# Optimization experiments

Measured on AMD Instinct MI355X. Metric: run time of the kernel, lower is better.

Reference implementation:

```python
import jax, jax.numpy as jnp
import numpy as np
from jax import lax

B, L, H, F, K, NBINS, MAXLEN = 32, 256, 256, 256, 3, 256, 2048
EPS = 1e-5


def _conv1d(x, w, b):
    # x: [B, L, Cin], w: [K, Cin, Cout] (torch Conv1d 'same' padding = (K-1)//2)
    pad = (w.shape[0] - 1) // 2
    y = lax.conv_general_dilated(x, w, (1,), [(pad, pad)],
                                 dimension_numbers=('NWC', 'WIO', 'NWC'))
    return y + b


def _layernorm(x, g, b):
    m = jnp.mean(x, axis=-1, keepdims=True)
    v = jnp.var(x, axis=-1, keepdims=True)
    return (x - m) * lax.rsqrt(v + EPS) * g + b


def _variance_predictor(x, i, w1, b1, g1, be1, w2, b2, g2, be2, wl, bl, mask):
    # conv -> relu -> LN -> conv -> relu -> LN -> linear -> squeeze -> masked_fill
    h = _layernorm(jax.nn.relu(_conv1d(x, w1[i], b1[i])), g1[i], be1[i])
    h = _layernorm(jax.nn.relu(_conv1d(h, w2[i], b2[i])), g2[i], be2[i])
    out = (h @ wl[i] + bl[i])[..., 0]          # [B, L]
    return jnp.where(mask, 0.0, out)


def _length_regulate(x, duration, max_len):
    # Vectorized replacement for the per-token expand/cat loop:
    # cumsum offsets + parallel gather into a padded buffer.
    cum = jnp.cumsum(duration, axis=1)          # [B, L]
    mel_len = cum[:, -1]                        # [B]
    t = jnp.arange(max_len)                     # [T]
    # phoneme index owning frame t: first position where cum > t
    idx = jax.vmap(lambda c: jnp.searchsorted(c, t, side='right'))(cum)  # [B, T]
    idx = jnp.minimum(idx, x.shape[1] - 1)
    out = jnp.take_along_axis(x, idx[:, :, None], axis=1)  # [B, T, H]
    valid = t[None, :] < mel_len[:, None]                   # [B, T]
    out = out * valid[:, :, None].astype(x.dtype)           # zero padding
    return out, mel_len, ~valid


def setup_inputs() -> dict:
    key = jax.random.key(0)
    ks = jax.random.split(key, 20)
    s = 1.0 / np.sqrt(H)
    inp = {
        'x': jax.random.normal(ks[0], (B, L, H), jnp.float32),
        'pitch_target': jax.random.normal(ks[1], (B, L), jnp.float32),
        'energy_target': jax.random.normal(ks[2], (B, L), jnp.float32),
        # stacked params for the 3 predictors: 0=duration, 1=pitch, 2=energy
        'w1': jax.random.normal(ks[3], (3, K, H, F), jnp.float32) * s,
        'b1': jnp.zeros((3, F), jnp.float32),
        'g1': jnp.ones((3, F), jnp.float32),
        'be1': jnp.zeros((3, F), jnp.float32),
        'w2': jax.random.normal(ks[4], (3, K, F, F), jnp.float32) * s,
        'b2': jnp.zeros((3, F), jnp.float32),
        'g2': jnp.ones((3, F), jnp.float32),
        'be2': jnp.zeros((3, F), jnp.float32),
        'wl': jax.random.normal(ks[5], (3, F, 1), jnp.float32) * s,
        'bl': jnp.zeros((3, 1), jnp.float32),
        'pitch_bins': jnp.linspace(-3.0, 3.0, NBINS - 1, dtype=jnp.float32),
        'energy_bins': jnp.linspace(-3.0, 3.0, NBINS - 1, dtype=jnp.float32),
        'pitch_emb': jax.random.normal(ks[6], (NBINS, H), jnp.float32),
        'energy_emb': jax.random.normal(ks[7], (NBINS, H), jnp.float32),
        'src_mask': jnp.zeros((B, L), bool),
        'duration_target': jax.random.randint(ks[8], (B, L), 0, 8),
        'max_len': MAXLEN,
    }
    return inp


def reference(x, pitch_target, energy_target,
              w1, b1, g1, be1, w2, b2, g2, be2, wl, bl,
              pitch_bins, energy_bins, pitch_emb, energy_emb,
              src_mask, duration_target, max_len):
    p = (w1, b1, g1, be1, w2, b2, g2, be2, wl, bl)
    log_duration_prediction = _variance_predictor(x, 0, *p, src_mask)
    # phoneme-level pitch (training path: target given -> bucketize + embed)
    pitch_prediction = _variance_predictor(x, 1, *p, src_mask)
    pitch_idx = jnp.searchsorted(pitch_bins, pitch_target, side='left')
    x = x + pitch_emb[pitch_idx]
    # phoneme-level energy (predictor sees x AFTER pitch embedding added)
    energy_prediction = _variance_predictor(x, 2, *p, src_mask)
    energy_idx = jnp.searchsorted(energy_bins, energy_target, side='left')
    x = x + energy_emb[energy_idx]
    # length regulator: duration_rounded = duration_target in training
    out, mel_len, mel_mask = _length_regulate(x, duration_target, max_len)
    return out, log_duration_prediction, pitch_prediction, energy_prediction, mel_len, mel_mask
```

## Files before the change

### kernel.cpp

```cpp
#include <hip/hip_runtime.h>
#include <hip/hip_bf16.h>
#include <cstdint>

typedef float f32x4 __attribute__((ext_vector_type(4)));
typedef short bf16x8 __attribute__((ext_vector_type(8)));

#define P_TOT 8192
#define KH 768
#define PADL 258
#define EPS_ 1e-5f

__device__ __forceinline__ unsigned short f2bf(float f) {
    unsigned int x = __float_as_uint(f);
    unsigned int r = (x + 0x7fffu + ((x >> 16) & 1u)) >> 16;
    return (unsigned short)r;
}

__global__ __launch_bounds__(256) void k_pre(
        const float* __restrict__ x, const float* __restrict__ pt, const float* __restrict__ et,
        const float* __restrict__ pbins, const float* __restrict__ ebins,
        const float* __restrict__ pemb, const float* __restrict__ eemb,
        const float* __restrict__ w1, const float* __restrict__ w2,
        const int* __restrict__ dur,
        unsigned short* __restrict__ xplain, unsigned short* __restrict__ xpplain,
        unsigned short* __restrict__ bt,
        float* __restrict__ out, float* __restrict__ maskout, float* __restrict__ mel_len_out) {
    __shared__ char smem[16640];
    const int bx = blockIdx.x;
    const int t = threadIdx.x;

    if (bx < 2048) {
        float* pb = (float*)smem;
        float* eb = pb + 256;
        int*   sc = (int*)(eb + 256);
        const int b = bx >> 6;
        if (t < 255) { pb[t] = pbins[t]; eb[t] = ebins[t]; }
        sc[t] = dur[b * 256 + t];
        for (int s = 1; s < 256; s <<= 1) {
            __syncthreads();
            int add = (t >= s) ? sc[t - s] : 0;
            __syncthreads();
            sc[t] += add;
        }
        __syncthreads();

        int w = t >> 6, lane = t & 63;
        int p = bx * 4 + w; int l = p & 255;
        float ptv = pt[p], etv = et[p];
        int lo = 0, hi = 255;
        while (lo < hi) { int mid = (lo + hi) >> 1; if (pb[mid] < ptv) lo = mid + 1; else hi = mid; }
        int pidx = lo;
        lo = 0; hi = 255;
        while (lo < hi) { int mid = (lo + hi) >> 1; if (eb[mid] < etv) lo = mid + 1; else hi = mid; }
        int eidx = lo;
        f32x4 xv = *(const f32x4*)(x    + (size_t)p * 256 + lane * 4);
        f32x4 pe = *(const f32x4*)(pemb + (size_t)pidx * 256 + lane * 4);
        f32x4 ee = *(const f32x4*)(eemb + (size_t)eidx * 256 + lane * 4);
        f32x4 xpv = xv + pe;
        f32x4 xpev = xpv + ee;
        size_t row = (size_t)b * PADL + 1 + l;
        ushort4 xb, xpb;
        xb.x = f2bf(xv[0]);  xb.y = f2bf(xv[1]);  xb.z = f2bf(xv[2]);  xb.w = f2bf(xv[3]);
        xpb.x = f2bf(xpv[0]); xpb.y = f2bf(xpv[1]); xpb.z = f2bf(xpv[2]); xpb.w = f2bf(xpv[3]);
        *(ushort4*)(xplain  + row * 256 + lane * 4) = xb;
        *(ushort4*)(xpplain + row * 256 + lane * 4) = xpb;
        ushort4 z; z.x = z.y = z.z = z.w = 0;
        if (l == 0) {
            *(ushort4*)(xplain  + ((size_t)b * PADL) * 256 + lane * 4) = z;
            *(ushort4*)(xpplain + ((size_t)b * PADL) * 256 + lane * 4) = z;
        }
        if (l == 255) {
            *(ushort4*)(xplain  + ((size_t)b * PADL + 257) * 256 + lane * 4) = z;
            *(ushort4*)(xpplain + ((size_t)b * PADL + 257) * 256 + lane * 4) = z;
        }
        int start = l ? sc[l - 1] : 0;
        int end = sc[l];
        for (int tt = start; tt < end; ++tt)
            *(f32x4*)(out + ((size_t)(b * 2048 + tt)) * 256 + lane * 4) = xpev;
    } else if (bx < 2336) {
        float (*tile)[65] = (float(*)[65])smem;
        int id = bx - 2048;
        int tf = id & 3; int th = (id >> 2) & 3;
        int rest = id >> 4;
        int k = rest % 3; rest /= 3;
        int set = rest % 3; int tensor = rest / 3;
        const float* src = tensor ? w2 : w1;
        const float* s = src + (((size_t)set * 3 + k) * 256 + th * 64) * 256 + tf * 64;
        int fl = t & 63;
        int q = t >> 6;
#pragma unroll
        for (int i = 0; i < 16; ++i) {
            int hl = i * 4 + q;
            tile[hl][fl] = s[(size_t)hl * 256 + fl];
        }
        __syncthreads();
        size_t rowbase = (size_t)tensor * 768 + set * 256 + tf * 64;
        size_t colbase = (size_t)k * 256 + th * 64;
#pragma unroll
        for (int i = 0; i < 16; ++i) {
            int f2 = i * 4 + q;
            bt[(rowbase + f2) * KH + colbase + fl] = f2bf(tile[fl][f2]);
        }
    } else if (bx < 2368) {
        int* sh = (int*)smem;
        int b = bx - 2336;
        sh[t] = dur[b * 256 + t];
        __syncthreads();
        for (int s = 128; s > 0; s >>= 1) {
            if (t < s) sh[t] += sh[t + s];
            __syncthreads();
        }
        if (t == 0) mel_len_out[b] = (float)sh[0];
    } else {
        int* sh = (int*)smem;
        int g = bx - 2368;
        int b = g >> 6;
        int t0 = (g & 63) * 32;
        sh[t] = dur[b * 256 + t];
        __syncthreads();
        for (int s = 128; s > 0; s >>= 1) {
            if (t < s) sh[t] += sh[t + s];
            __syncthreads();
        }
        int mel = sh[0];
        int w = t >> 6, lane = t & 63;
        f32x4 z4 = (f32x4){0.f, 0.f, 0.f, 0.f};
#pragma unroll
        for (int it = 0; it < 8; ++it) {
            int tt = t0 + it * 4 + w;
            if (tt >= mel)
                *(f32x4*)(out + ((size_t)(b * 2048 + tt)) * 256 + lane * 4) = z4;
        }
        if (t < 32) maskout[b * 2048 + t0 + t] = (t0 + t < mel) ? 0.f : 1.f;
    }
}

__device__ __forceinline__ void stageA128(const unsigned short* __restrict__ A, int browPad,
                                          unsigned short* As, int tid) {
    for (int g = tid; g < 4160; g += 512) {
        int p = g * 16;
        int r = p >> 9;
        int c = (p & 511) ^ ((r & 7) << 4);
        __builtin_amdgcn_global_load_lds(
            (const __attribute__((address_space(1))) unsigned int*)((const char*)(A + (size_t)(browPad + r) * 256) + c),
            (__attribute__((address_space(3))) unsigned int*)((char*)As + p), 16, 0, 0);
    }
}

__device__ __forceinline__ void stageB128(const unsigned short* __restrict__ Bm, int kt,
                                          unsigned short* Bs, int tid) {
#pragma unroll
    for (int j = 0; j < 2; ++j) {
        int p = j * 8192 + tid * 16;
        int c = p >> 6;
        int kb = (p & 63) ^ ((c & 3) << 4);
        __builtin_amdgcn_global_load_lds(
            (const __attribute__((address_space(1))) unsigned int*)((const char*)(Bm + (size_t)c * KH + kt) + kb),
            (__attribute__((address_space(3))) unsigned int*)((char*)Bs + p), 16, 0, 0);
    }
}

__device__ __forceinline__ void compute128(const unsigned short* As, const unsigned short* Bs,
                                           int kt, int lane, int wr, int wc, f32x4 acc[4][4]) {
    const int rsel = lane & 15;
    const int lhi = lane >> 4;
    const int tap = kt >> 8;
    const int hcb = (kt & 255) * 2 + lhi * 16;
    bf16x8 af[4], bfr[4];
#pragma unroll
    for (int m = 0; m < 4; ++m) {
        int r = tap + wr * 64 + m * 16 + rsel;
        af[m] = *(const bf16x8*)((const char*)As + r * 512 + (hcb ^ ((r & 7) << 4)));
    }
#pragma unroll
    for (int n = 0; n < 4; ++n) {
        int c = wc * 64 + n * 16 + rsel;
        bfr[n] = *(const bf16x8*)((const char*)Bs + c * 64 + ((lhi * 16) ^ ((c & 3) << 4)));
    }
#pragma unroll
    for (int m = 0; m < 4; ++m)
#pragma unroll
        for (int n = 0; n < 4; ++n)
            acc[m][n] = __builtin_amdgcn_mfma_f32_16x16x32_bf16(af[m], bfr[n], acc[m][n], 0, 0, 0);
}

__global__ __launch_bounds__(512) void k_conv_ln1(
        const unsigned short* __restrict__ xplain, const unsigned short* __restrict__ xpplain,
        const unsigned short* __restrict__ bt,
        const float* __restrict__ b1, const float* __restrict__ g1, const float* __restrict__ be1,
        unsigned short* __restrict__ h0, unsigned short* __restrict__ h1, unsigned short* __restrict__ h2) {
    __shared__ unsigned short As[33280];
    __shared__ unsigned short Bs[2][8192];
    __shared__ float2 red[4][128];

    const int pred = blockIdx.y;
    const unsigned short* A  = (pred < 2) ? xplain : xpplain;
    const unsigned short* Bm = bt + (size_t)pred * 256 * KH;
    unsigned short* hout = (pred == 0) ? h0 : (pred == 1) ? h1 : h2;

    const int rowBase = blockIdx.x * 128;
    const int bb = rowBase >> 8;
    const int l0 = rowBase & 255;
    const int browPad = bb * PADL + l0;
    const int tid = threadIdx.x;
    const int lane = tid & 63;
    const int wv = tid >> 6;
    const int wr = wv >> 2, wc = wv & 3;
    const int rsel = lane & 15;
    const int lhi = lane >> 4;

    f32x4 acc[4][4];
#pragma unroll
    for (int m = 0; m < 4; ++m)
#pragma unroll
        for (int n = 0; n < 4; ++n) acc[m][n] = (f32x4){0.f, 0.f, 0.f, 0.f};

    stageA128(A, browPad, As, tid);
    stageB128(Bm, 0, Bs[0], tid);
    __syncthreads();
    int cur = 0;
    for (int kt = 32; kt < KH; kt += 32) {
        stageB128(Bm, kt, Bs[cur ^ 1], tid);
        compute128(As, Bs[cur], kt - 32, lane, wr, wc, acc);
        __syncthreads();
        cur ^= 1;
    }
    compute128(As, Bs[cur], KH - 32, lane, wr, wc, acc);

    float bcol[4], gcol[4], becol[4];
#pragma unroll
    for (int n = 0; n < 4; ++n) {
        int c = wc * 64 + n * 16 + rsel;
        bcol[n] = b1[pred * 256 + c];
        gcol[n] = g1[pred * 256 + c];
        becol[n] = be1[pred * 256 + c];
    }

#pragma unroll
    for (int m = 0; m < 4; ++m)
#pragma unroll
        for (int r = 0; r < 4; ++r) {
            float s = 0.f, s2 = 0.f;
#pragma unroll
            for (int n = 0; n < 4; ++n) {
                float v = fmaxf(acc[m][n][r] + bcol[n], 0.f);
                s += v; s2 += v * v;
            }
#pragma unroll
            for (int o = 1; o < 16; o <<= 1) { s += __shfl_xor(s, o); s2 += __shfl_xor(s2, o); }
            if (rsel == 0) red[wc][wr * 64 + m * 16 + lhi * 4 + r] = make_float2(s, s2);
        }
    __syncthreads();
    if (tid < 128) {
        float2 a0 = red[0][tid], a1 = red[1][tid], a2 = red[2][tid], a3 = red[3][tid];
        red[0][tid] = make_float2(a0.x + a1.x + a2.x + a3.x, a0.y + a1.y + a2.y + a3.y);
    }
    __syncthreads();

#pragma unroll
    for (int m = 0; m < 4; ++m)
#pragma unroll
        for (int r = 0; r < 4; ++r) {
            int rl = wr * 64 + m * 16 + lhi * 4 + r;
            float2 t = red[0][rl];
            float mean = t.x * (1.f / 256.f);
            float var = t.y * (1.f / 256.f) - mean * mean;
            float inv = rsqrtf(var + EPS_);
            int l = l0 + rl;
            size_t row = (size_t)bb * PADL + 1 + l;
#pragma unroll
            for (int n = 0; n < 4; ++n) {
                float v = fmaxf(acc[m][n][r] + bcol[n], 0.f);
                float h = (v - mean) * inv * gcol[n] + becol[n];
                int c = wc * 64 + n * 16 + rsel;
                hout[row * 256 + c] = f2bf(h);
                if (l == 0)   hout[((size_t)bb * PADL) * 256 + c] = 0;
                if (l == 255) hout[((size_t)bb * PADL + 257) * 256 + c] = 0;
            }
        }
}

__global__ __launch_bounds__(512) void k_conv_ln2(
        const unsigned short* __restrict__ h0, const unsigned short* __restrict__ h1,
        const unsigned short* __restrict__ h2, const unsigned short* __restrict__ bt,
        const float* __restrict__ b2, const float* __restrict__ g2, const float* __restrict__ be2,
        const float* __restrict__ wl, const float* __restrict__ bl,
        const char* __restrict__ mask, float* __restrict__ outp) {
    __shared__ unsigned short As[33280];
    __shared__ unsigned short Bs[2][8192];
    __shared__ float2 red[4][128];
    __shared__ float  red2[4][128];

    const int pred = blockIdx.y;
    const unsigned short* A  = (pred == 0) ? h0 : (pred == 1) ? h1 : h2;
    const unsigned short* Bm = bt + (size_t)(768 + pred * 256) * KH;

    const int rowBase = blockIdx.x * 128;
    const int bb = rowBase >> 8;
    const int l0 = rowBase & 255;
    const int browPad = bb * PADL + l0;
    const int tid = threadIdx.x;
    const int lane = tid & 63;
    const int wv = tid >> 6;
    const int wr = wv >> 2, wc = wv & 3;
    const int rsel = lane & 15;
    const int lhi = lane >> 4;

    f32x4 acc[4][4];
#pragma unroll
    for (int m = 0; m < 4; ++m)
#pragma unroll
        for (int n = 0; n < 4; ++n) acc[m][n] = (f32x4){0.f, 0.f, 0.f, 0.f};

    stageA128(A, browPad, As, tid);
    stageB128(Bm, 0, Bs[0], tid);
    __syncthreads();
    int cur = 0;
    for (int kt = 32; kt < KH; kt += 32) {
        stageB128(Bm, kt, Bs[cur ^ 1], tid);
        compute128(As, Bs[cur], kt - 32, lane, wr, wc, acc);
        __syncthreads();
        cur ^= 1;
    }
    compute128(As, Bs[cur], KH - 32, lane, wr, wc, acc);

    float bcol[4], gcol[4], becol[4], wcol[4];
#pragma unroll
    for (int n = 0; n < 4; ++n) {
        int c = wc * 64 + n * 16 + rsel;
        bcol[n] = b2[pred * 256 + c];
        gcol[n] = g2[pred * 256 + c];
        becol[n] = be2[pred * 256 + c];
        wcol[n] = wl[pred * 256 + c];
    }

#pragma unroll
    for (int m = 0; m < 4; ++m)
#pragma unroll
        for (int r = 0; r < 4; ++r) {
            float s = 0.f, s2 = 0.f;
#pragma unroll
            for (int n = 0; n < 4; ++n) {
                float v = fmaxf(acc[m][n][r] + bcol[n], 0.f);
                s += v; s2 += v * v;
            }
#pragma unroll
            for (int o = 1; o < 16; o <<= 1) { s += __shfl_xor(s, o); s2 += __shfl_xor(s2, o); }
            if (rsel == 0) red[wc][wr * 64 + m * 16 + lhi * 4 + r] = make_float2(s, s2);
        }
    __syncthreads();
    if (tid < 128) {
        float2 a0 = red[0][tid], a1 = red[1][tid], a2 = red[2][tid], a3 = red[3][tid];
        red[0][tid] = make_float2(a0.x + a1.x + a2.x + a3.x, a0.y + a1.y + a2.y + a3.y);
    }
    __syncthreads();

#pragma unroll
    for (int m = 0; m < 4; ++m)
#pragma unroll
        for (int r = 0; r < 4; ++r) {
            int rl = wr * 64 + m * 16 + lhi * 4 + r;
            float2 t = red[0][rl];
            float mean = t.x * (1.f / 256.f);
            float var = t.y * (1.f / 256.f) - mean * mean;
            float inv = rsqrtf(var + EPS_);
            float d = 0.f;
#pragma unroll
            for (int n = 0; n < 4; ++n) {
                float v = fmaxf(acc[m][n][r] + bcol[n], 0.f);
                float h = (v - mean) * inv * gcol[n] + becol[n];
                d += h * wcol[n];
            }
#pragma unroll
            for (int o = 1; o < 16; o <<= 1) d += __shfl_xor(d, o);
            if (rsel == 0) red2[wc][rl] = d;
        }
    __syncthreads();
    if (tid < 128) {
        int p = rowBase + tid;
        float o = red2[0][tid] + red2[1][tid] + red2[2][tid] + red2[3][tid] + bl[pred];
        if (mask[p]) o = 0.f;
        outp[(size_t)pred * P_TOT + p] = o;
    }
}

extern "C" void kernel_launch(void* const* d_in, const int* in_sizes, int n_in,
                              void* d_out, int out_size, void* d_ws, size_t ws_size,
                              hipStream_t stream) {
    const float* x     = (const float*)d_in[0];
    const float* pt    = (const float*)d_in[1];
    const float* et    = (const float*)d_in[2];
    const float* w1    = (const float*)d_in[3];
    const float* b1    = (const float*)d_in[4];
    const float* g1    = (const float*)d_in[5];
    const float* be1   = (const float*)d_in[6];
    const float* w2    = (const float*)d_in[7];
    const float* b2    = (const float*)d_in[8];
    const float* g2    = (const float*)d_in[9];
    const float* be2   = (const float*)d_in[10];
    const float* wl    = (const float*)d_in[11];
    const float* bl    = (const float*)d_in[12];
    const float* pbins = (const float*)d_in[13];
    const float* ebins = (const float*)d_in[14];
    const float* pemb  = (const float*)d_in[15];
    const float* eemb  = (const float*)d_in[16];
    const char*  mask  = (const char*)d_in[17];
    const int*   dur   = (const int*)d_in[18];

    char* ws = (char*)d_ws;
    unsigned short* xplain  = (unsigned short*)(ws + 0);
    unsigned short* xpplain = (unsigned short*)(ws + 8388608);
    unsigned short* h0      = (unsigned short*)(ws + 16777216);
    unsigned short* h1      = (unsigned short*)(ws + 25165824);
    unsigned short* h2      = (unsigned short*)(ws + 33554432);
    unsigned short* btall   = (unsigned short*)(ws + 52428800);

    float* out        = (float*)d_out;
    float* out_pred   = out + 16777216;
    float* out_mellen = out + 16801792;
    float* out_mask   = out + 16801824;

    hipLaunchKernelGGL(k_pre, dim3(4416), dim3(256), 0, stream,
                       x, pt, et, pbins, ebins, pemb, eemb, w1, w2, dur,
                       xplain, xpplain, btall, out, out_mask, out_mellen);

    hipLaunchKernelGGL(k_conv_ln1, dim3(64, 3), dim3(512), 0, stream,
                       xplain, xpplain, btall, b1, g1, be1, h0, h1, h2);

    hipLaunchKernelGGL(k_conv_ln2, dim3(64, 3), dim3(512), 0, stream,
                       h0, h1, h2, btall, b2, g2, be2, wl, bl, mask, out_pred);
}
```

Measured before the change: 73.87 us.

## Triple-buffer weight tiles with vmcnt-based waits in conv K-loop

Replaces the double-buffered B staging with a three-stage ring buffer, so weight tiles are prefetched two iterations ahead. Each step waits on an explicit s_waitcnt vmcnt and a single s_barrier in place of a full __syncthreads. The goal is to hide global-load latency behind the MFMA work. The cost is 16 KB more LDS per block, which may lower occupancy. Correctness depends on the vmcnt count matching the number of loads stageB128 issues per thread.

```diff
diff --git a/kernel.cpp b/kernel.cpp
--- a/kernel.cpp
+++ b/kernel.cpp
@@ -184,13 +184,34 @@
             acc[m][n] = __builtin_amdgcn_mfma_f32_16x16x32_bf16(af[m], bfr[n], acc[m][n], 0, 0, 0);
 }
 
+__device__ __forceinline__ void conv_kloop(const unsigned short* __restrict__ A,
+                                           const unsigned short* __restrict__ Bm,
+                                           int browPad, int lane, int wr, int wc, int tid,
+                                           unsigned short* As, unsigned short (*Bs)[8192],
+                                           f32x4 acc[4][4]) {
+    stageB128(Bm, 0, Bs[0], tid);
+    stageA128(A, browPad, As, tid);
+    stageB128(Bm, 32, Bs[1], tid);
+#pragma unroll
+    for (int t = 0; t < 24; ++t) {
+        if (t <= 21) asm volatile("s_waitcnt vmcnt(2)" ::: "memory");
+        else         asm volatile("s_waitcnt vmcnt(0)" ::: "memory");
+        __builtin_amdgcn_s_barrier();
+        __builtin_amdgcn_sched_barrier(0);
+        if (t + 2 < 24)
+            stageB128(Bm, (t + 2) * 32, Bs[(t + 2) % 3], tid);
+        compute128(As, Bs[t % 3], t * 32, lane, wr, wc, acc);
+    }
+    __syncthreads();
+}
+
 __global__ __launch_bounds__(512) void k_conv_ln1(
         const unsigned short* __restrict__ xplain, const unsigned short* __restrict__ xpplain,
         const unsigned short* __restrict__ bt,
         const float* __restrict__ b1, const float* __restrict__ g1, const float* __restrict__ be1,
         unsigned short* __restrict__ h0, unsigned short* __restrict__ h1, unsigned short* __restrict__ h2) {
     __shared__ unsigned short As[33280];
-    __shared__ unsigned short Bs[2][8192];
+    __shared__ unsigned short Bs[3][8192];
     __shared__ float2 red[4][128];
 
     const int pred = blockIdx.y;
@@ -215,17 +236,7 @@
 #pragma unroll
         for (int n = 0; n < 4; ++n) acc[m][n] = (f32x4){0.f, 0.f, 0.f, 0.f};
 
-    stageA128(A, browPad, As, tid);
-    stageB128(Bm, 0, Bs[0], tid);
-    __syncthreads();
-    int cur = 0;
-    for (int kt = 32; kt < KH; kt += 32) {
-        stageB128(Bm, kt, Bs[cur ^ 1], tid);
-        compute128(As, Bs[cur], kt - 32, lane, wr, wc, acc);
-        __syncthreads();
-        cur ^= 1;
-    }
-    compute128(As, Bs[cur], KH - 32, lane, wr, wc, acc);
+    conv_kloop(A, Bm, browPad, lane, wr, wc, tid, As, Bs, acc);
 
     float bcol[4], gcol[4], becol[4];
 #pragma unroll
@@ -287,7 +298,7 @@
         const float* __restrict__ wl, const float* __restrict__ bl,
         const char* __restrict__ mask, float* __restrict__ outp) {
     __shared__ unsigned short As[33280];
-    __shared__ unsigned short Bs[2][8192];
+    __shared__ unsigned short Bs[3][8192];
     __shared__ float2 red[4][128];
     __shared__ float  red2[4][128];
 
@@ -312,17 +323,7 @@
 #pragma unroll
         for (int n = 0; n < 4; ++n) acc[m][n] = (f32x4){0.f, 0.f, 0.f, 0.f};
 
-    stageA128(A, browPad, As, tid);
-    stageB128(Bm, 0, Bs[0], tid);
-    __syncthreads();
-    int cur = 0;
-    for (int kt = 32; kt < KH; kt += 32) {
-        stageB128(Bm, kt, Bs[cur ^ 1], tid);
-        compute128(As, Bs[cur], kt - 32, lane, wr, wc, acc);
-        __syncthreads();
-        cur ^= 1;
-    }
-    compute128(As, Bs[cur], KH - 32, lane, wr, wc, acc);
+    conv_kloop(A, Bm, browPad, lane, wr, wc, tid, As, Bs, acc);
 
     float bcol[4], gcol[4], becol[4], wcol[4];
 #pragma unroll
```

Result: faster. 63.87 us (-13.5%).
